# Performance work log

Measured on AMD Instinct MI355X. Metric: run time of the kernel, lower is better.

## Reference

```python
import jax, jax.numpy as jnp
import numpy as np

B, N, D = 4, 4096, 512
K = 16384          # codebook size
NUM_Q = 2          # residual quantizers (shared codebook)


def setup_inputs() -> dict:
    key = jax.random.key(0)
    ks = jax.random.split(key, 6)
    s = 1.0 / np.sqrt(D)
    return {
        "x": jax.random.normal(ks[0], (B, N, D), dtype=jnp.float32),
        "enc_w": jax.random.normal(ks[1], (D, D), dtype=jnp.float32) * s,
        "enc_b": jnp.zeros((D,), dtype=jnp.float32),
        "codebook": jax.random.normal(ks[2], (K, D), dtype=jnp.float32),
        "dec_w": jax.random.normal(ks[3], (D, D), dtype=jnp.float32) * s,
        "dec_b": jnp.zeros((D,), dtype=jnp.float32),
    }


def _residual_vq(z, codebook):
    # z: [B, N, D] -> flatten tokens
    flat = z.reshape(-1, z.shape[-1])          # [T, D]
    c_sq = jnp.sum(codebook * codebook, axis=-1)  # [K]
    q_sum = jnp.zeros_like(flat)
    residual = flat
    for _ in range(NUM_Q):
        # argmin of ||r - c||^2 == argmin of (||c||^2 - 2 r.c); skip ||r||^2
        dists = c_sq[None, :] - 2.0 * (residual @ codebook.T)  # [T, K]
        idx = jnp.argmin(dists, axis=-1)                       # [T]
        q = codebook[idx]                                      # gather [T, D]
        q_sum = q_sum + q
        residual = residual - q
    return q_sum.reshape(z.shape)


def reference(x, enc_w, enc_b, codebook, dec_w, dec_b):
    z = x @ enc_w.T + enc_b                     # encoder Linear(512 -> 512)
    q = _residual_vq(z, codebook)               # sum of per-stage code vectors
    z_tilde = z + jax.lax.stop_gradient(q - z)  # straight-through estimator
    x_recon = z_tilde @ dec_w.T + dec_b         # decoder Linear(512 -> 512)
    return x_recon
```

## Files before the change

kernel.cpp:

```cpp
#include <hip/hip_runtime.h>
#include <stdint.h>

constexpr int TT = 16384;
constexpr int DD = 512;
constexpr int KK = 16384;
constexpr int TOPK = 8;

constexpr int BM = 128, BN = 128, BK = 32;
constexpr int PAD = 4;
constexpr int LDW = BN + PAD;

typedef __bf16 bf16x8 __attribute__((ext_vector_type(8)));
typedef __bf16 bf16x4 __attribute__((ext_vector_type(4)));
typedef float f32x4 __attribute__((ext_vector_type(4)));

typedef const __attribute__((address_space(1))) void* gas_ptr;
typedef __attribute__((address_space(3))) void* las_ptr;

__device__ __forceinline__ unsigned long long pack_di(float d, int idx) {
    uint32_t u = __float_as_uint(d);
    u = (u & 0x80000000u) ? ~u : (u | 0x80000000u);
    return ((unsigned long long)u << 32) | (uint32_t)idx;
}

__device__ __forceinline__ unsigned long long umin64(unsigned long long a,
                                                     unsigned long long b) {
    return a < b ? a : b;
}

template<int MODE>
__global__ __launch_bounds__(256)
void gemm512(const float* __restrict__ A, const float* __restrict__ A2,
             const float* __restrict__ W, const float* __restrict__ bias,
             float* __restrict__ out0, float* __restrict__ out1,
             __bf16* __restrict__ out2, int N)
{
    __shared__ float As[BK][LDW];
    __shared__ float Bs[BK][LDW];
    const int tid = threadIdx.x;
    const int tx = tid & 15, ty = tid >> 4;
    const int row0 = blockIdx.y * BM;
    const int col0 = blockIdx.x * BN;
    const int r4 = tid >> 3;
    const int c4 = tid & 7;

    float acc[8][8] = {};

    for (int kb = 0; kb < DD; kb += BK) {
        #pragma unroll
        for (int p = 0; p < 4; ++p) {
            const int row = p * 32 + r4;
            float4 v = *(const float4*)(A + (size_t)(row0 + row) * DD + kb + c4 * 4);
            if (MODE == 1) {
                const float4 w = *(const float4*)(A2 + (size_t)(row0 + row) * DD + kb + c4 * 4);
                v.x -= w.x; v.y -= w.y; v.z -= w.z; v.w -= w.w;
            }
            As[c4*4+0][row] = v.x; As[c4*4+1][row] = v.y;
            As[c4*4+2][row] = v.z; As[c4*4+3][row] = v.w;
        }
        #pragma unroll
        for (int p = 0; p < 4; ++p) {
            const int col = p * 32 + r4;
            const float4 v = *(const float4*)(W + (size_t)(col0 + col) * DD + kb + c4 * 4);
            Bs[c4*4+0][col] = v.x; Bs[c4*4+1][col] = v.y;
            Bs[c4*4+2][col] = v.z; Bs[c4*4+3][col] = v.w;
        }
        __syncthreads();
        #pragma unroll
        for (int k = 0; k < BK; ++k) {
            float a[8], b[8];
            *(float4*)&a[0] = *(const float4*)&As[k][ty*8];
            *(float4*)&a[4] = *(const float4*)&As[k][ty*8+4];
            *(float4*)&b[0] = *(const float4*)&Bs[k][tx*8];
            *(float4*)&b[4] = *(const float4*)&Bs[k][tx*8+4];
            #pragma unroll
            for (int i = 0; i < 8; ++i)
                #pragma unroll
                for (int j = 0; j < 8; ++j)
                    acc[i][j] += a[i] * b[j];
        }
        __syncthreads();
    }

    #pragma unroll
    for (int i = 0; i < 8; ++i) {
        const int row = row0 + ty*8 + i;
        #pragma unroll
        for (int j = 0; j < 8; j += 4) {
            const int col = col0 + tx*8 + j;
            float4 o;
            o.x = acc[i][j+0] + bias[col+0];
            o.y = acc[i][j+1] + bias[col+1];
            o.z = acc[i][j+2] + bias[col+2];
            o.w = acc[i][j+3] + bias[col+3];
            *(float4*)(out0 + (size_t)row * N + col) = o;
            if (MODE == 0) {
                *(float4*)(out1 + (size_t)row * N + col) = o;
                bf16x4 h; h[0] = (__bf16)o.x; h[1] = (__bf16)o.y;
                h[2] = (__bf16)o.z; h[3] = (__bf16)o.w;
                *(bf16x4*)(out2 + (size_t)row * N + col) = h;
            }
        }
    }
}

__global__ __launch_bounds__(256)
void cvt_bf16(const float* __restrict__ src, __bf16* __restrict__ dst)
{
    const size_t g = ((size_t)blockIdx.x * 256 + threadIdx.x) * 8;
    const float4 a = *(const float4*)(src + g);
    const float4 b = *(const float4*)(src + g + 4);
    bf16x8 h;
    h[0] = (__bf16)a.x; h[1] = (__bf16)a.y; h[2] = (__bf16)a.z; h[3] = (__bf16)a.w;
    h[4] = (__bf16)b.x; h[5] = (__bf16)b.y; h[6] = (__bf16)b.z; h[7] = (__bf16)b.w;
    *(bf16x8*)(dst + g) = h;
}

__global__ __launch_bounds__(256)
void dist_approx(const __bf16* __restrict__ Rh,
                 const __bf16* __restrict__ Ch,
                 const float* __restrict__ csq,
                 unsigned long long* __restrict__ winners)
{
    __shared__ __bf16 As[128 * 32];
    __shared__ __bf16 Bs[128 * 32];
    const int tid = threadIdx.x;
    const int lane = tid & 63;
    const int w = tid >> 6;
    const int row0 = blockIdx.y * 128;
    const int col0 = blockIdx.x * 128;

    f32x4 acc[2][8] = {};

    const int srow0 = w * 32 + (lane >> 2);
    const int srow1 = srow0 + 16;
    const int gc0 = (lane & 3) ^ ((srow0 >> 1) & 3);
    const int gc1 = (lane & 3) ^ ((srow1 >> 1) & 3);
    __bf16* ldsA0 = As + (w * 32 + 0) * 32;
    __bf16* ldsA1 = As + (w * 32 + 16) * 32;
    __bf16* ldsB0 = Bs + (w * 32 + 0) * 32;
    __bf16* ldsB1 = Bs + (w * 32 + 16) * 32;

    int a_off[2], b_off[8];
    #pragma unroll
    for (int mi = 0; mi < 2; ++mi) {
        const int ar = w * 32 + mi * 16 + (lane & 15);
        a_off[mi] = ar * 32 + (((lane >> 4) ^ ((ar >> 1) & 3)) << 3);
    }
    #pragma unroll
    for (int ni = 0; ni < 8; ++ni) {
        const int br = ni * 16 + (lane & 15);
        b_off[ni] = br * 32 + (((lane >> 4) ^ ((br >> 1) & 3)) << 3);
    }

    for (int kb = 0; kb < 512; kb += 32) {
        __syncthreads();
        __builtin_amdgcn_global_load_lds(
            (gas_ptr)(Rh + (size_t)(row0 + srow0) * 512 + kb + gc0 * 8), (las_ptr)ldsA0, 16, 0, 0);
        __builtin_amdgcn_global_load_lds(
            (gas_ptr)(Rh + (size_t)(row0 + srow1) * 512 + kb + gc1 * 8), (las_ptr)ldsA1, 16, 0, 0);
        __builtin_amdgcn_global_load_lds(
            (gas_ptr)(Ch + (size_t)(col0 + srow0) * 512 + kb + gc0 * 8), (las_ptr)ldsB0, 16, 0, 0);
        __builtin_amdgcn_global_load_lds(
            (gas_ptr)(Ch + (size_t)(col0 + srow1) * 512 + kb + gc1 * 8), (las_ptr)ldsB1, 16, 0, 0);
        __syncthreads();

        bf16x8 af[2], bfr[8];
        #pragma unroll
        for (int mi = 0; mi < 2; ++mi) af[mi] = *(const bf16x8*)(As + a_off[mi]);
        #pragma unroll
        for (int ni = 0; ni < 8; ++ni) bfr[ni] = *(const bf16x8*)(Bs + b_off[ni]);
        #pragma unroll
        for (int mi = 0; mi < 2; ++mi)
            #pragma unroll
            for (int ni = 0; ni < 8; ++ni)
                acc[mi][ni] = __builtin_amdgcn_mfma_f32_16x16x32_bf16(
                    af[mi], bfr[ni], acc[mi][ni], 0, 0, 0);
    }

    float csv[8];
    #pragma unroll
    for (int ni = 0; ni < 8; ++ni)
        csv[ni] = csq[col0 + ni * 16 + (lane & 15)];

    #pragma unroll
    for (int mi = 0; mi < 2; ++mi) {
        #pragma unroll
        for (int reg = 0; reg < 4; ++reg) {
            unsigned long long b = ~0ull, s = ~0ull;
            #pragma unroll
            for (int ni = 0; ni < 8; ++ni) {
                const float d = fmaf(-2.0f, acc[mi][ni][reg], csv[ni]);
                const unsigned long long x = pack_di(d, col0 + ni * 16 + (lane & 15));
                const unsigned long long nb = umin64(b, x);
                s = umin64(s, b ^ x ^ nb);
                b = nb;
            }
            #pragma unroll
            for (int m = 1; m < 16; m <<= 1) {
                const unsigned long long ob = __shfl_xor(b, m, 16);
                const unsigned long long os = __shfl_xor(s, m, 16);
                const unsigned long long nb = umin64(b, ob);
                s = umin64(umin64(s, os), b ^ ob ^ nb);
                b = nb;
            }
            if ((lane & 15) == 0) {
                const int row = row0 + w * 32 + mi * 16 + (lane >> 4) * 4 + reg;
                winners[(size_t)row * 256 + blockIdx.x * 2 + 0] = b;
                winners[(size_t)row * 256 + blockIdx.x * 2 + 1] = s;
            }
        }
    }
}

__global__ __launch_bounds__(256)
void select_rescore(const unsigned long long* __restrict__ winners,
                    const float* __restrict__ CB, const float* __restrict__ csq,
                    float* __restrict__ R, __bf16* __restrict__ R16)
{
    const int w = threadIdx.x >> 6;
    const int lane = threadIdx.x & 63;
    const int token = blockIdx.x * 4 + w;

    const unsigned long long* wt = winners + (size_t)token * 256;
    unsigned long long v[4];
    #pragma unroll
    for (int j = 0; j < 4; ++j) v[j] = wt[lane * 4 + j];

    unsigned long long cand[TOPK];
    #pragma unroll
    for (int t = 0; t < TOPK; ++t) {
        unsigned long long mm = umin64(umin64(v[0], v[1]), umin64(v[2], v[3]));
        #pragma unroll
        for (int m = 1; m < 64; m <<= 1)
            mm = umin64(mm, __shfl_xor(mm, m, 64));
        cand[t] = mm;
        #pragma unroll
        for (int j = 0; j < 4; ++j) if (v[j] == mm) v[j] = ~0ull;
    }

    float4 r0 = *(const float4*)(R + (size_t)token * 512 + lane * 8);
    float4 r1 = *(const float4*)(R + (size_t)token * 512 + lane * 8 + 4);

    unsigned long long best = ~0ull;
    #pragma unroll
    for (int t = 0; t < TOPK; ++t) {
        const int col = (int)(cand[t] & 0xFFFFFFFFull);
        const float4 c0 = *(const float4*)(CB + (size_t)col * 512 + lane * 8);
        const float4 c1 = *(const float4*)(CB + (size_t)col * 512 + lane * 8 + 4);
        float dot = r0.x * c0.x;
        dot = fmaf(r0.y, c0.y, dot); dot = fmaf(r0.z, c0.z, dot);
        dot = fmaf(r0.w, c0.w, dot); dot = fmaf(r1.x, c1.x, dot);
        dot = fmaf(r1.y, c1.y, dot); dot = fmaf(r1.z, c1.z, dot);
        dot = fmaf(r1.w, c1.w, dot);
        #pragma unroll
        for (int m = 1; m < 64; m <<= 1) dot += __shfl_xor(dot, m, 64);
        const float d = fmaf(-2.0f, dot, csq[col]);
        best = umin64(best, pack_di(d, col));
    }

    const int bcol = (int)(best & 0xFFFFFFFFull);
    const float4 c0 = *(const float4*)(CB + (size_t)bcol * 512 + lane * 8);
    const float4 c1 = *(const float4*)(CB + (size_t)bcol * 512 + lane * 8 + 4);
    r0.x -= c0.x; r0.y -= c0.y; r0.z -= c0.z; r0.w -= c0.w;
    r1.x -= c1.x; r1.y -= c1.y; r1.z -= c1.z; r1.w -= c1.w;
    *(float4*)(R + (size_t)token * 512 + lane * 8) = r0;
    *(float4*)(R + (size_t)token * 512 + lane * 8 + 4) = r1;
    bf16x8 h;
    h[0] = (__bf16)r0.x; h[1] = (__bf16)r0.y; h[2] = (__bf16)r0.z; h[3] = (__bf16)r0.w;
    h[4] = (__bf16)r1.x; h[5] = (__bf16)r1.y; h[6] = (__bf16)r1.z; h[7] = (__bf16)r1.w;
    *(bf16x8*)(R16 + (size_t)token * 512 + lane * 8) = h;
}

__global__ __launch_bounds__(256)
void csq_kernel(const float* __restrict__ CB, float* __restrict__ c_sq)
{
    const int wave = threadIdx.x >> 6;
    const int lane = threadIdx.x & 63;
    const int row = blockIdx.x * 4 + wave;
    const float* p = CB + (size_t)row * DD + lane * 8;
    const float4 a = *(const float4*)p;
    const float4 b = *(const float4*)(p + 4);
    float s = a.x*a.x + a.y*a.y + a.z*a.z + a.w*a.w
            + b.x*b.x + b.y*b.y + b.z*b.z + b.w*b.w;
    #pragma unroll
    for (int m = 1; m < 64; m <<= 1) s += __shfl_xor(s, m, 64);
    if (lane == 0) c_sq[row] = s;
}

extern "C" void kernel_launch(void* const* d_in, const int* in_sizes, int n_in,
                              void* d_out, int out_size, void* d_ws, size_t ws_size,
                              hipStream_t stream)
{
    const float* x    = (const float*)d_in[0];
    const float* encw = (const float*)d_in[1];
    const float* encb = (const float*)d_in[2];
    const float* cb   = (const float*)d_in[3];
    const float* decw = (const float*)d_in[4];
    const float* decb = (const float*)d_in[5];
    float* out = (float*)d_out;

    float* z    = (float*)d_ws;
    float* r    = z + (size_t)TT * DD;
    __bf16* cb16 = (__bf16*)(r + (size_t)TT * DD);
    __bf16* r16  = cb16 + (size_t)KK * DD;
    float* csq  = (float*)(r16 + (size_t)TT * DD);
    unsigned long long* winners = (unsigned long long*)d_out;

    const dim3 blk(256);

    gemm512<0><<<dim3(DD / BN, TT / BM), blk, 0, stream>>>(
        x, nullptr, encw, encb, z, r, r16, DD);

    csq_kernel<<<dim3(KK / 4), blk, 0, stream>>>(cb, csq);
    cvt_bf16<<<dim3(KK * DD / 8 / 256), blk, 0, stream>>>(cb, cb16);

    for (int s = 0; s < 2; ++s) {
        dist_approx<<<dim3(KK / 128, TT / 128), blk, 0, stream>>>(r16, cb16, csq, winners);
        select_rescore<<<dim3(TT / 4), blk, 0, stream>>>(winners, cb, csq, r, r16);
    }

    gemm512<1><<<dim3(DD / BN, TT / BM), blk, 0, stream>>>(
        z, r, decw, decb, out, nullptr, nullptr, DD);
}
```

Before: 1.218 ms.

## Use split-bf16 MFMA for linear layers, widen distance K-tile, fuse codebook prep

Replaces the scalar FP32 encoder/decoder GEMMs with MFMA kernels that split each FP32 operand into bf16 high and low parts and run three bf16 MFMAs to approximate FP32 accuracy. The distance kernel's K-step grows from 32 to 64 with a new XOR swizzle, halving the barrier and load rounds. The codebook bf16 conversion is fused into the norm kernel, removing one launch and one read of the codebook. Risks include reduced precision in the linear layers, possible LDS bank conflicts with the new swizzle, and uncoalesced scalar epilogue stores.

```diff
diff --git a/kernel.cpp b/kernel.cpp
--- a/kernel.cpp
+++ b/kernel.cpp
@@ -6,10 +6,6 @@
 constexpr int KK = 16384;
 constexpr int TOPK = 8;
 
-constexpr int BM = 128, BN = 128, BK = 32;
-constexpr int PAD = 4;
-constexpr int LDW = BN + PAD;
-
 typedef __bf16 bf16x8 __attribute__((ext_vector_type(8)));
 typedef __bf16 bf16x4 __attribute__((ext_vector_type(4)));
 typedef float f32x4 __attribute__((ext_vector_type(4)));
@@ -30,90 +26,103 @@
 
 template<int MODE>
 __global__ __launch_bounds__(256)
-void gemm512(const float* __restrict__ A, const float* __restrict__ A2,
-             const float* __restrict__ W, const float* __restrict__ bias,
-             float* __restrict__ out0, float* __restrict__ out1,
-             __bf16* __restrict__ out2, int N)
-{
-    __shared__ float As[BK][LDW];
-    __shared__ float Bs[BK][LDW];
+void gemm_mfma(const float* __restrict__ A, const float* __restrict__ A2,
+               const float* __restrict__ W, const float* __restrict__ bias,
+               float* __restrict__ out0, float* __restrict__ out1,
+               __bf16* __restrict__ out2)
+{
+    __shared__ __bf16 Ah[128 * 64], Al[128 * 64];
+    __shared__ __bf16 Bh[128 * 64], Bl[128 * 64];
     const int tid = threadIdx.x;
-    const int tx = tid & 15, ty = tid >> 4;
-    const int row0 = blockIdx.y * BM;
-    const int col0 = blockIdx.x * BN;
-    const int r4 = tid >> 3;
-    const int c4 = tid & 7;
-
-    float acc[8][8] = {};
-
-    for (int kb = 0; kb < DD; kb += BK) {
-        #pragma unroll
-        for (int p = 0; p < 4; ++p) {
-            const int row = p * 32 + r4;
-            float4 v = *(const float4*)(A + (size_t)(row0 + row) * DD + kb + c4 * 4);
+    const int lane = tid & 63;
+    const int w = tid >> 6;
+    const int row0 = blockIdx.y * 128;
+    const int col0 = blockIdx.x * 128;
+
+    f32x4 acc[2][8] = {};
+
+    const int sr = tid >> 4;
+    const int scol = (tid & 15) * 4;
+    const int lcol = (((scol >> 3) ^ (sr & 7)) << 3) + (scol & 7);
+
+    int a_off[2], b_off[8];
+    #pragma unroll
+    for (int mi = 0; mi < 2; ++mi) {
+        const int ar = w * 32 + mi * 16 + (lane & 15);
+        a_off[mi] = ar * 64 + (((lane >> 4) ^ (lane & 7)) << 3);
+    }
+    #pragma unroll
+    for (int ni = 0; ni < 8; ++ni) {
+        const int br = ni * 16 + (lane & 15);
+        b_off[ni] = br * 64 + (((lane >> 4) ^ (lane & 7)) << 3);
+    }
+
+    for (int kb = 0; kb < 512; kb += 64) {
+        __syncthreads();
+        #pragma unroll
+        for (int i = 0; i < 8; ++i) {
+            const int r = i * 16 + sr;
+            float4 v = *(const float4*)(A + (size_t)(row0 + r) * 512 + kb + scol);
             if (MODE == 1) {
-                const float4 w = *(const float4*)(A2 + (size_t)(row0 + row) * DD + kb + c4 * 4);
-                v.x -= w.x; v.y -= w.y; v.z -= w.z; v.w -= w.w;
-            }
-            As[c4*4+0][row] = v.x; As[c4*4+1][row] = v.y;
-            As[c4*4+2][row] = v.z; As[c4*4+3][row] = v.w;
-        }
-        #pragma unroll
-        for (int p = 0; p < 4; ++p) {
-            const int col = p * 32 + r4;
-            const float4 v = *(const float4*)(W + (size_t)(col0 + col) * DD + kb + c4 * 4);
-            Bs[c4*4+0][col] = v.x; Bs[c4*4+1][col] = v.y;
-            Bs[c4*4+2][col] = v.z; Bs[c4*4+3][col] = v.w;
+                const float4 u = *(const float4*)(A2 + (size_t)(row0 + r) * 512 + kb + scol);
+                v.x -= u.x; v.y -= u.y; v.z -= u.z; v.w -= u.w;
+            }
+            bf16x4 hv, lv;
+            hv[0] = (__bf16)v.x; hv[1] = (__bf16)v.y; hv[2] = (__bf16)v.z; hv[3] = (__bf16)v.w;
+            lv[0] = (__bf16)(v.x - (float)hv[0]); lv[1] = (__bf16)(v.y - (float)hv[1]);
+            lv[2] = (__bf16)(v.z - (float)hv[2]); lv[3] = (__bf16)(v.w - (float)hv[3]);
+            *(bf16x4*)(Ah + r * 64 + lcol) = hv;
+            *(bf16x4*)(Al + r * 64 + lcol) = lv;
+
+            const float4 x = *(const float4*)(W + (size_t)(col0 + r) * 512 + kb + scol);
+            bf16x4 hw, lw;
+            hw[0] = (__bf16)x.x; hw[1] = (__bf16)x.y; hw[2] = (__bf16)x.z; hw[3] = (__bf16)x.w;
+            lw[0] = (__bf16)(x.x - (float)hw[0]); lw[1] = (__bf16)(x.y - (float)hw[1]);
+            lw[2] = (__bf16)(x.z - (float)hw[2]); lw[3] = (__bf16)(x.w - (float)hw[3]);
+            *(bf16x4*)(Bh + r * 64 + lcol) = hw;
+            *(bf16x4*)(Bl + r * 64 + lcol) = lw;
         }
         __syncthreads();
         #pragma unroll
-        for (int k = 0; k < BK; ++k) {
-            float a[8], b[8];
-            *(float4*)&a[0] = *(const float4*)&As[k][ty*8];
-            *(float4*)&a[4] = *(const float4*)&As[k][ty*8+4];
-            *(float4*)&b[0] = *(const float4*)&Bs[k][tx*8];
-            *(float4*)&b[4] = *(const float4*)&Bs[k][tx*8+4];
-            #pragma unroll
-            for (int i = 0; i < 8; ++i)
+        for (int s = 0; s < 2; ++s) {
+            const int sx = s * 32;
+            bf16x8 ah[2], al[2];
+            #pragma unroll
+            for (int mi = 0; mi < 2; ++mi) {
+                ah[mi] = *(const bf16x8*)(Ah + (a_off[mi] ^ sx));
+                al[mi] = *(const bf16x8*)(Al + (a_off[mi] ^ sx));
+            }
+            #pragma unroll
+            for (int ni = 0; ni < 8; ++ni) {
+                const bf16x8 bh = *(const bf16x8*)(Bh + (b_off[ni] ^ sx));
+                const bf16x8 bl = *(const bf16x8*)(Bl + (b_off[ni] ^ sx));
                 #pragma unroll
-                for (int j = 0; j < 8; ++j)
-                    acc[i][j] += a[i] * b[j];
-        }
-        __syncthreads();
-    }
-
-    #pragma unroll
-    for (int i = 0; i < 8; ++i) {
-        const int row = row0 + ty*8 + i;
-        #pragma unroll
-        for (int j = 0; j < 8; j += 4) {
-            const int col = col0 + tx*8 + j;
-            float4 o;
-            o.x = acc[i][j+0] + bias[col+0];
-            o.y = acc[i][j+1] + bias[col+1];
-            o.z = acc[i][j+2] + bias[col+2];
-            o.w = acc[i][j+3] + bias[col+3];
-            *(float4*)(out0 + (size_t)row * N + col) = o;
-            if (MODE == 0) {
-                *(float4*)(out1 + (size_t)row * N + col) = o;
-                bf16x4 h; h[0] = (__bf16)o.x; h[1] = (__bf16)o.y;
-                h[2] = (__bf16)o.z; h[3] = (__bf16)o.w;
-                *(bf16x4*)(out2 + (size_t)row * N + col) = h;
-            }
-        }
-    }
-}
-
-__global__ __launch_bounds__(256)
-void cvt_bf16(const float* __restrict__ src, __bf16* __restrict__ dst)
-{
-    const size_t g = ((size_t)blockIdx.x * 256 + threadIdx.x) * 8;
-    const float4 a = *(const float4*)(src + g);
-    const float4 b = *(const float4*)(src + g + 4);
-    bf16x8 h;
-    h[0] = (__bf16)a.x; h[1] = (__bf16)a.y; h[2] = (__bf16)a.z; h[3] = (__bf16)a.w;
-    h[4] = (__bf16)b.x; h[5] = (__bf16)b.y; h[6] = (__bf16)b.z; h[7] = (__bf16)b.w;
-    *(bf16x8*)(dst + g) = h;
+                for (int mi = 0; mi < 2; ++mi) {
+                    acc[mi][ni] = __builtin_amdgcn_mfma_f32_16x16x32_bf16(ah[mi], bh, acc[mi][ni], 0, 0, 0);
+                    acc[mi][ni] = __builtin_amdgcn_mfma_f32_16x16x32_bf16(ah[mi], bl, acc[mi][ni], 0, 0, 0);
+                    acc[mi][ni] = __builtin_amdgcn_mfma_f32_16x16x32_bf16(al[mi], bh, acc[mi][ni], 0, 0, 0);
+                }
+            }
+        }
+    }
+
+    #pragma unroll
+    for (int mi = 0; mi < 2; ++mi) {
+        #pragma unroll
+        for (int reg = 0; reg < 4; ++reg) {
+            const int row = row0 + w * 32 + mi * 16 + (lane >> 4) * 4 + reg;
+            #pragma unroll
+            for (int ni = 0; ni < 8; ++ni) {
+                const int col = col0 + ni * 16 + (lane & 15);
+                const float o = acc[mi][ni][reg] + bias[col];
+                out0[(size_t)row * 512 + col] = o;
+                if (MODE == 0) {
+                    out1[(size_t)row * 512 + col] = o;
+                    out2[(size_t)row * 512 + col] = (__bf16)o;
+                }
+            }
+        }
+    }
 }
 
 __global__ __launch_bounds__(256)
@@ -122,8 +131,8 @@
                  const float* __restrict__ csq,
                  unsigned long long* __restrict__ winners)
 {
-    __shared__ __bf16 As[128 * 32];
-    __shared__ __bf16 Bs[128 * 32];
+    __shared__ __bf16 As[128 * 64];
+    __shared__ __bf16 Bs[128 * 64];
     const int tid = threadIdx.x;
     const int lane = tid & 63;
     const int w = tid >> 6;
@@ -132,50 +141,49 @@
 
     f32x4 acc[2][8] = {};
 
-    const int srow0 = w * 32 + (lane >> 2);
-    const int srow1 = srow0 + 16;
-    const int gc0 = (lane & 3) ^ ((srow0 >> 1) & 3);
-    const int gc1 = (lane & 3) ^ ((srow1 >> 1) & 3);
-    __bf16* ldsA0 = As + (w * 32 + 0) * 32;
-    __bf16* ldsA1 = As + (w * 32 + 16) * 32;
-    __bf16* ldsB0 = Bs + (w * 32 + 0) * 32;
-    __bf16* ldsB1 = Bs + (w * 32 + 16) * 32;
+    const int gc = (lane & 7) ^ ((lane >> 3) & 7);
+    const __bf16* Ab = Rh + (size_t)(row0 + w * 32 + (lane >> 3)) * 512 + gc * 8;
+    const __bf16* Bb = Ch + (size_t)(col0 + w * 32 + (lane >> 3)) * 512 + gc * 8;
+    __bf16* lA = As + (w * 32) * 64;
+    __bf16* lB = Bs + (w * 32) * 64;
 
     int a_off[2], b_off[8];
     #pragma unroll
     for (int mi = 0; mi < 2; ++mi) {
         const int ar = w * 32 + mi * 16 + (lane & 15);
-        a_off[mi] = ar * 32 + (((lane >> 4) ^ ((ar >> 1) & 3)) << 3);
+        a_off[mi] = ar * 64 + (((lane >> 4) ^ (lane & 7)) << 3);
     }
     #pragma unroll
     for (int ni = 0; ni < 8; ++ni) {
         const int br = ni * 16 + (lane & 15);
-        b_off[ni] = br * 32 + (((lane >> 4) ^ ((br >> 1) & 3)) << 3);
-    }
-
-    for (int kb = 0; kb < 512; kb += 32) {
+        b_off[ni] = br * 64 + (((lane >> 4) ^ (lane & 7)) << 3);
+    }
+
+    for (int kb = 0; kb < 512; kb += 64) {
         __syncthreads();
-        __builtin_amdgcn_global_load_lds(
-            (gas_ptr)(Rh + (size_t)(row0 + srow0) * 512 + kb + gc0 * 8), (las_ptr)ldsA0, 16, 0, 0);
-        __builtin_amdgcn_global_load_lds(
-            (gas_ptr)(Rh + (size_t)(row0 + srow1) * 512 + kb + gc1 * 8), (las_ptr)ldsA1, 16, 0, 0);
-        __builtin_amdgcn_global_load_lds(
-            (gas_ptr)(Ch + (size_t)(col0 + srow0) * 512 + kb + gc0 * 8), (las_ptr)ldsB0, 16, 0, 0);
-        __builtin_amdgcn_global_load_lds(
-            (gas_ptr)(Ch + (size_t)(col0 + srow1) * 512 + kb + gc1 * 8), (las_ptr)ldsB1, 16, 0, 0);
+        #pragma unroll
+        for (int j = 0; j < 4; ++j) {
+            __builtin_amdgcn_global_load_lds(
+                (gas_ptr)(Ab + (size_t)j * 8 * 512 + kb), (las_ptr)(lA + j * 8 * 64), 16, 0, 0);
+            __builtin_amdgcn_global_load_lds(
+                (gas_ptr)(Bb + (size_t)j * 8 * 512 + kb), (las_ptr)(lB + j * 8 * 64), 16, 0, 0);
+        }
         __syncthreads();
-
-        bf16x8 af[2], bfr[8];
-        #pragma unroll
-        for (int mi = 0; mi < 2; ++mi) af[mi] = *(const bf16x8*)(As + a_off[mi]);
-        #pragma unroll
-        for (int ni = 0; ni < 8; ++ni) bfr[ni] = *(const bf16x8*)(Bs + b_off[ni]);
-        #pragma unroll
-        for (int mi = 0; mi < 2; ++mi)
-            #pragma unroll
-            for (int ni = 0; ni < 8; ++ni)
-                acc[mi][ni] = __builtin_amdgcn_mfma_f32_16x16x32_bf16(
-                    af[mi], bfr[ni], acc[mi][ni], 0, 0, 0);
+        #pragma unroll
+        for (int s = 0; s < 2; ++s) {
+            const int sx = s * 32;
+            bf16x8 af[2], bfr[8];
+            #pragma unroll
+            for (int mi = 0; mi < 2; ++mi) af[mi] = *(const bf16x8*)(As + (a_off[mi] ^ sx));
+            #pragma unroll
+            for (int ni = 0; ni < 8; ++ni) bfr[ni] = *(const bf16x8*)(Bs + (b_off[ni] ^ sx));
+            #pragma unroll
+            for (int mi = 0; mi < 2; ++mi)
+                #pragma unroll
+                for (int ni = 0; ni < 8; ++ni)
+                    acc[mi][ni] = __builtin_amdgcn_mfma_f32_16x16x32_bf16(
+                        af[mi], bfr[ni], acc[mi][ni], 0, 0, 0);
+        }
     }
 
     float csv[8];
@@ -273,7 +281,8 @@
 }
 
 __global__ __launch_bounds__(256)
-void csq_kernel(const float* __restrict__ CB, float* __restrict__ c_sq)
+void prep_cb(const float* __restrict__ CB, float* __restrict__ c_sq,
+             __bf16* __restrict__ cb16)
 {
     const int wave = threadIdx.x >> 6;
     const int lane = threadIdx.x & 63;
@@ -281,6 +290,10 @@
     const float* p = CB + (size_t)row * DD + lane * 8;
     const float4 a = *(const float4*)p;
     const float4 b = *(const float4*)(p + 4);
+    bf16x8 h;
+    h[0] = (__bf16)a.x; h[1] = (__bf16)a.y; h[2] = (__bf16)a.z; h[3] = (__bf16)a.w;
+    h[4] = (__bf16)b.x; h[5] = (__bf16)b.y; h[6] = (__bf16)b.z; h[7] = (__bf16)b.w;
+    *(bf16x8*)(cb16 + (size_t)row * DD + lane * 8) = h;
     float s = a.x*a.x + a.y*a.y + a.z*a.z + a.w*a.w
             + b.x*b.x + b.y*b.y + b.z*b.z + b.w*b.w;
     #pragma unroll
@@ -309,17 +322,16 @@
 
     const dim3 blk(256);
 
-    gemm512<0><<<dim3(DD / BN, TT / BM), blk, 0, stream>>>(
-        x, nullptr, encw, encb, z, r, r16, DD);
-
-    csq_kernel<<<dim3(KK / 4), blk, 0, stream>>>(cb, csq);
-    cvt_bf16<<<dim3(KK * DD / 8 / 256), blk, 0, stream>>>(cb, cb16);
+    gemm_mfma<0><<<dim3(DD / 128, TT / 128), blk, 0, stream>>>(
+        x, nullptr, encw, encb, z, r, r16);
+
+    prep_cb<<<dim3(KK / 4), blk, 0, stream>>>(cb, csq, cb16);
 
     for (int s = 0; s < 2; ++s) {
         dist_approx<<<dim3(KK / 128, TT / 128), blk, 0, stream>>>(r16, cb16, csq, winners);
         select_rescore<<<dim3(TT / 4), blk, 0, stream>>>(winners, cb, csq, r, r16);
     }
 
-    gemm512<1><<<dim3(DD / BN, TT / BM), blk, 0, stream>>>(
-        z, r, decw, decb, out, nullptr, nullptr, DD);
-}
+    gemm_mfma<1><<<dim3(DD / 128, TT / 128), blk, 0, stream>>>(
+        z, r, decw, decb, out, nullptr, nullptr);
+}
```

New measurement: 1.126 ms. 1.08x faster.
